# Kernel optimization log

Hardware: AMD Instinct MI355X
Metric: run time of the kernel (lower is better)

## Reference

```python
import jax, jax.numpy as jnp
import numpy as np

VOCAB, EMB, HID, LAT = 32000, 512, 1024, 64
B, S = 64, 512

def setup_inputs() -> dict:
    key = jax.random.key(0)
    ks = jax.random.split(key, 10)
    s_e = 1.0 / np.sqrt(HID)
    s_l = 1.0 / np.sqrt(HID)
    return {
        'input_ids': jax.random.randint(ks[0], (B, S), 0, VOCAB),
        'emb_weight': jax.random.normal(ks[1], (VOCAB, EMB), jnp.float32),
        'w_ih': jax.random.uniform(ks[2], (3 * HID, EMB), jnp.float32, -s_e, s_e),
        'w_hh': jax.random.uniform(ks[3], (3 * HID, HID), jnp.float32, -s_e, s_e),
        'b_ih': jax.random.uniform(ks[4], (3 * HID,), jnp.float32, -s_e, s_e),
        'b_hh': jax.random.uniform(ks[5], (3 * HID,), jnp.float32, -s_e, s_e),
        'w_mean': jax.random.uniform(ks[6], (LAT, HID), jnp.float32, -s_l, s_l),
        'b_mean': jax.random.uniform(ks[7], (LAT,), jnp.float32, -s_l, s_l),
        'w_logv': jax.random.uniform(ks[8], (LAT, HID), jnp.float32, -s_l, s_l),
        'b_logv': jax.random.uniform(ks[9], (LAT,), jnp.float32, -s_l, s_l),
    }

def _gru_mean_hidden(ids, emb_weight, w_ih, w_hh, b_ih, b_hh):
    x = emb_weight[ids]                      # [B, S, E]
    # precompute input-side gate preactivations for all timesteps
    gx = jnp.einsum('bse,ge->bsg', x, w_ih) + b_ih   # [B, S, 3H]
    gx_t = jnp.swapaxes(gx, 0, 1)            # [S, B, 3H] for scan

    def step(h, gx_i):
        gh = h @ w_hh.T + b_hh               # [B, 3H]
        # torch GRU gate order: r, z, n
        r = jax.nn.sigmoid(gx_i[:, :HID] + gh[:, :HID])
        z = jax.nn.sigmoid(gx_i[:, HID:2 * HID] + gh[:, HID:2 * HID])
        n = jnp.tanh(gx_i[:, 2 * HID:] + r * gh[:, 2 * HID:])
        h_new = (1.0 - z) * n + z * h
        return h_new, h_new

    h0 = jnp.zeros((ids.shape[0], HID), gx.dtype)
    _, hs = jax.lax.scan(step, h0, gx_t)      # hs: [S, B, H]
    return jnp.mean(hs, axis=0)               # mean pooling over time -> [B, H]

def reference(input_ids, emb_weight, w_ih, w_hh, b_ih, b_hh, w_mean, b_mean, w_logv, b_logv):
    h = _gru_mean_hidden(input_ids, emb_weight, w_ih, w_hh, b_ih, b_hh)
    mean = h @ w_mean.T + b_mean
    logv = h @ w_logv.T + b_logv
    return (mean, logv)
```

## Files before the change

### kernel.cpp

```cpp
#include <hip/hip_runtime.h>
#include <hip/hip_bf16.h>
#include <stdint.h>
#include <stddef.h>

#define HID   1024
#define NB    64
#define SEQ   512
#define G3    3072
#define EMB   512
#define LAT   64

typedef __attribute__((ext_vector_type(4))) float f32x4;
typedef __attribute__((ext_vector_type(8))) short bfrag;
typedef unsigned long long ull;

__device__ __forceinline__ unsigned short f2bf(float x) {
  union { float f; unsigned u; } v; v.f = x;
  unsigned u = v.u + 0x7fffu + ((v.u >> 16) & 1u);
  return (unsigned short)(u >> 16);
}
__device__ __forceinline__ float bf2f(short s) {
  union { unsigned u; float f; } v; v.u = ((unsigned)(unsigned short)s) << 16;
  return v.f;
}
__device__ __forceinline__ float fsig(float x) {
  return 1.0f / (1.0f + __builtin_exp2f(-1.4426950408889634f * x));
}
__device__ __forceinline__ float ftanh(float x) {
  return 1.0f - 2.0f / (1.0f + __builtin_exp2f(2.8853900817779268f * x));
}
__device__ __forceinline__ void gload_lds16(const void* g, void* l) {
  __builtin_amdgcn_global_load_lds(
      (const __attribute__((address_space(1))) unsigned int*)g,
      (__attribute__((address_space(3))) unsigned int*)l, 16, 0, 0);
}

__global__ void cvt_wih_kernel(const float* __restrict__ in, short* __restrict__ out) {
  int i = (blockIdx.x * 256 + threadIdx.x) * 8;
  f32x4 a = *(const f32x4*)(in + i);
  f32x4 b = *(const f32x4*)(in + i + 4);
  bfrag o;
  o[0]=(short)f2bf(a[0]); o[1]=(short)f2bf(a[1]); o[2]=(short)f2bf(a[2]); o[3]=(short)f2bf(a[3]);
  o[4]=(short)f2bf(b[0]); o[5]=(short)f2bf(b[1]); o[6]=(short)f2bf(b[2]); o[7]=(short)f2bf(b[3]);
  *(bfrag*)(out + i) = o;
}

__global__ void __launch_bounds__(256) gemm_gx_kernel(
    const int* __restrict__ ids, const float* __restrict__ emb,
    const short* __restrict__ wih, short* __restrict__ gx)
{
  const int nt = blockIdx.x, mt = blockIdx.y;
  const int tid = threadIdx.x;
  const int lane = tid & 63, wave = tid >> 6;
  const int wr = wave >> 1, wc = wave & 1;

  __shared__ __align__(16) short A_lds[128 * 48];
  __shared__ __align__(16) short B_lds[128 * 32];
  __shared__ int ids_s[128];

  if (tid < 128) ids_s[tid] = ids[mt * 128 + tid];
  __syncthreads();

  f32x4 acc[4][4];
  #pragma unroll
  for (int i = 0; i < 4; ++i)
    #pragma unroll
    for (int j = 0; j < 4; ++j) acc[i][j] = (f32x4){0.f, 0.f, 0.f, 0.f};

  const int r_stage = tid >> 1;
  const int kh = (tid & 1) * 16;

  #pragma unroll 1
  for (int kc = 0; kc < 16; ++kc) {
    __syncthreads();
    {
      const float* src = emb + (size_t)ids_s[r_stage] * 512 + kc * 32 + kh;
      f32x4 v0 = *(const f32x4*)(src);
      f32x4 v1 = *(const f32x4*)(src + 4);
      f32x4 v2 = *(const f32x4*)(src + 8);
      f32x4 v3 = *(const f32x4*)(src + 12);
      bfrag p0, p1;
      p0[0]=(short)f2bf(v0[0]); p0[1]=(short)f2bf(v0[1]); p0[2]=(short)f2bf(v0[2]); p0[3]=(short)f2bf(v0[3]);
      p0[4]=(short)f2bf(v1[0]); p0[5]=(short)f2bf(v1[1]); p0[6]=(short)f2bf(v1[2]); p0[7]=(short)f2bf(v1[3]);
      p1[0]=(short)f2bf(v2[0]); p1[1]=(short)f2bf(v2[1]); p1[2]=(short)f2bf(v2[2]); p1[3]=(short)f2bf(v2[3]);
      p1[4]=(short)f2bf(v3[0]); p1[5]=(short)f2bf(v3[1]); p1[6]=(short)f2bf(v3[2]); p1[7]=(short)f2bf(v3[3]);
      *(bfrag*)&A_lds[r_stage * 48 + kh]     = p0;
      *(bfrag*)&A_lds[r_stage * 48 + kh + 8] = p1;
    }
    {
      #pragma unroll
      for (int ii = 0; ii < 2; ++ii) {
        int i = wave * 2 + ii;
        const short* src = wih + (size_t)(nt * 128 + i * 16 + (lane >> 2)) * 512
                               + kc * 32 + (lane & 3) * 8;
        gload_lds16((const void*)src, (void*)&B_lds[i * 512]);
      }
    }
    asm volatile("s_waitcnt vmcnt(0)" ::: "memory");
    __syncthreads();

    bfrag a[4], b[4];
    #pragma unroll
    for (int mi = 0; mi < 4; ++mi)
      a[mi] = *(const bfrag*)&A_lds[(wr * 64 + mi * 16 + (lane & 15)) * 48 + (lane >> 4) * 8];
    #pragma unroll
    for (int ni = 0; ni < 4; ++ni)
      b[ni] = *(const bfrag*)&B_lds[(wc * 64 + ni * 16 + (lane & 15)) * 32 + (lane >> 4) * 8];
    #pragma unroll
    for (int mi = 0; mi < 4; ++mi)
      #pragma unroll
      for (int ni = 0; ni < 4; ++ni)
        acc[mi][ni] = __builtin_amdgcn_mfma_f32_16x16x32_bf16(a[mi], b[ni], acc[mi][ni], 0, 0, 0);
  }

  #pragma unroll
  for (int mi = 0; mi < 4; ++mi)
    #pragma unroll
    for (int ni = 0; ni < 4; ++ni)
      #pragma unroll
      for (int r = 0; r < 4; ++r) {
        int m = mt * 128 + wr * 64 + mi * 16 + (lane >> 4) * 4 + r;
        int n = nt * 128 + wc * 64 + ni * 16 + (lane & 15);
        gx[(size_t)m * G3 + n] = (short)f2bf(acc[mi][ni][r]);
      }
}

__global__ void __launch_bounds__(256, 1) gru_scan_kernel(
    const short* __restrict__ gx, const float* __restrict__ whh,
    const float* __restrict__ bihp, const float* __restrict__ bhhp,
    ull* __restrict__ hbuf_q, unsigned int* __restrict__ flags,
    float* __restrict__ hsum)
{
  const int wg   = blockIdx.x;
  const int team = wg >> 6;
  const int cg   = wg & 63;
  const int tid  = threadIdx.x;
  const int lane = tid & 63, wave = tid >> 6;
  const int bl   = lane & 15;
  const int bsub = (lane >> 4) * 4;
  const int jcol = cg * 16 + bl;
  const int bteam = team * 16;

  __shared__ __align__(16) short h_lds[16 * 1024];
  __shared__ __align__(16) float part[3 * 3 * 256];
  __shared__ __align__(16) short hstg[256];

  bfrag wfrag[3][8];
  #pragma unroll
  for (int g = 0; g < 3; ++g) {
    const float* wrow = whh + (size_t)(g * 1024 + jcol) * 1024 + wave * 256 + (lane >> 4) * 8;
    #pragma unroll
    for (int ks = 0; ks < 8; ++ks) {
      const float* p = wrow + ks * 32;
      f32x4 lo = *(const f32x4*)p;
      f32x4 hi = *(const f32x4*)(p + 4);
      bfrag f;
      f[0]=(short)f2bf(lo[0]); f[1]=(short)f2bf(lo[1]); f[2]=(short)f2bf(lo[2]); f[3]=(short)f2bf(lo[3]);
      f[4]=(short)f2bf(hi[0]); f[5]=(short)f2bf(hi[1]); f[6]=(short)f2bf(hi[2]); f[7]=(short)f2bf(hi[3]);
      wfrag[g][ks] = f;
    }
  }
  float bih_r[3], bhh_r[3];
  #pragma unroll
  for (int g = 0; g < 3; ++g) {
    bih_r[g] = bihp[g * 1024 + jcol];
    bhh_r[g] = bhhp[g * 1024 + jcol];
  }

  float hprev[4] = {0.f, 0.f, 0.f, 0.f};
  float hacc[4]  = {0.f, 0.f, 0.f, 0.f};
  const int xorm = (bl & 7) << 4;
  const char* lbase = (const char*)h_lds + bl * 2048;
  unsigned int* fteam  = flags + team * 1024;
  unsigned int* myflag = fteam + cg * 16;
  unsigned int* fq     = fteam + (wave * 16 + (lane & 15)) * 16;

  const int st_b  = lane >> 2;
  const int st_c4 = lane & 3;
  char* const st_base = (char*)h_lds + st_b * 2048;
  const int st_swz = (st_b & 7) << 4;

  short gxr_[4][3];
  if (wave == 0) {
    #pragma unroll
    for (int r = 0; r < 4; ++r) {
      size_t base = ((size_t)(bteam + bsub + r) * SEQ + 0) * G3 + jcol;
      gxr_[r][0] = gx[base];
      gxr_[r][1] = gx[base + 1024];
      gxr_[r][2] = gx[base + 2048];
    }
  }

  #pragma unroll 1
  for (int s = 0; s < SEQ; ++s) {
    const ull* hsrc = hbuf_q + ((s & 1) ? 16384 : 0) + team * 4096;
    ull*       hdst = hbuf_q + (((s + 1) & 1) ? 16384 : 0) + team * 4096;

    {
      unsigned tgt = (unsigned)s;
      for (;;) {
        unsigned v = __hip_atomic_load(fq, __ATOMIC_RELAXED, __HIP_MEMORY_SCOPE_AGENT);
        if (__all((int)(v >= tgt))) break;
      }
    }

    {
      ull hv[16];
      #pragma unroll
      for (int j = 0; j < 16; ++j)
        hv[j] = __hip_atomic_load(hsrc + wave * 1024 + j * 64 + lane,
                                  __ATOMIC_RELAXED, __HIP_MEMORY_SCOPE_AGENT);
      #pragma unroll
      for (int j = 0; j < 16; ++j) {
        int cgq = wave * 16 + j;
        *(ull*)(st_base + ((cgq * 32 + st_c4 * 8) ^ st_swz)) = hv[j];
      }
    }

    f32x4 a0 = {0.f,0.f,0.f,0.f}, a1 = {0.f,0.f,0.f,0.f}, a2 = {0.f,0.f,0.f,0.f};
    #pragma unroll
    for (int ks = 0; ks < 8; ++ks) {
      int k2 = wave * 512 + ks * 64 + (lane >> 4) * 16;
      bfrag af = *(const bfrag*)(lbase + (k2 ^ xorm));
      a0 = __builtin_amdgcn_mfma_f32_16x16x32_bf16(af, wfrag[0][ks], a0, 0, 0, 0);
      a1 = __builtin_amdgcn_mfma_f32_16x16x32_bf16(af, wfrag[1][ks], a1, 0, 0, 0);
      a2 = __builtin_amdgcn_mfma_f32_16x16x32_bf16(af, wfrag[2][ks], a2, 0, 0, 0);
    }
    if (wave) {
      int w1 = wave - 1;
      *(f32x4*)&part[((0 * 3 + w1) * 64 + lane) * 4] = a0;
      *(f32x4*)&part[((1 * 3 + w1) * 64 + lane) * 4] = a1;
      *(f32x4*)&part[((2 * 3 + w1) * 64 + lane) * 4] = a2;
    }
    __syncthreads();

    if (wave == 0) {
      f32x4 s0 = a0, s1 = a1, s2 = a2;
      #pragma unroll
      for (int w1 = 0; w1 < 3; ++w1) {
        s0 += *(const f32x4*)&part[((0 * 3 + w1) * 64 + lane) * 4];
        s1 += *(const f32x4*)&part[((1 * 3 + w1) * 64 + lane) * 4];
        s2 += *(const f32x4*)&part[((2 * 3 + w1) * 64 + lane) * 4];
      }
      #pragma unroll
      for (int r = 0; r < 4; ++r) {
        float ghr = s0[r] + bhh_r[0];
        float ghz = s1[r] + bhh_r[1];
        float ghn = s2[r] + bhh_r[2];
        float rg = fsig(bf2f(gxr_[r][0]) + bih_r[0] + ghr);
        float zg = fsig(bf2f(gxr_[r][1]) + bih_r[1] + ghz);
        float ng = ftanh(bf2f(gxr_[r][2]) + bih_r[2] + rg * ghn);
        float hn = (1.f - zg) * ng + zg * hprev[r];
        hprev[r] = hn;
        hacc[r] += hn;
        hstg[(bsub + r) * 16 + bl] = (short)f2bf(hn);
      }
    }
    __syncthreads();

    if (wave == 1) {
      ull v = ((const ull*)hstg)[lane];
      __hip_atomic_store(hdst + cg * 64 + lane, v, __ATOMIC_RELAXED,
                         __HIP_MEMORY_SCOPE_AGENT);
      asm volatile("s_waitcnt vmcnt(0)" ::: "memory");
      if (lane == 0)
        __hip_atomic_store(myflag, (unsigned)(s + 1), __ATOMIC_RELAXED,
                           __HIP_MEMORY_SCOPE_AGENT);
    }
    if (wave == 0) {
      int sn = (s + 1 < SEQ) ? (s + 1) : s;
      #pragma unroll
      for (int r = 0; r < 4; ++r) {
        size_t base = ((size_t)(bteam + bsub + r) * SEQ + sn) * G3 + jcol;
        gxr_[r][0] = gx[base];
        gxr_[r][1] = gx[base + 1024];
        gxr_[r][2] = gx[base + 2048];
      }
    }
  }

  if (wave == 0) {
    #pragma unroll
    for (int r = 0; r < 4; ++r)
      hsum[(size_t)(bteam + bsub + r) * 1024 + jcol] = hacc[r] * (1.0f / 512.0f);
  }
}

__global__ void proj_kernel(const float* __restrict__ hbar,
                            const float* __restrict__ wm, const float* __restrict__ bm,
                            const float* __restrict__ wl, const float* __restrict__ bl,
                            float* __restrict__ out)
{
  int b = blockIdx.x, t = threadIdx.x;
  __shared__ float hrow[1024];
  for (int k = t; k < 1024; k += 128) hrow[k] = hbar[(size_t)b * 1024 + k];
  __syncthreads();
  int j = t & 63;
  const float* w = (t < 64) ? (wm + (size_t)j * 1024) : (wl + (size_t)j * 1024);
  float acc = (t < 64) ? bm[j] : bl[j];
  for (int k = 0; k < 1024; k += 4) {
    f32x4 wv = *(const f32x4*)(w + k);
    acc += hrow[k] * wv[0] + hrow[k+1] * wv[1] + hrow[k+2] * wv[2] + hrow[k+3] * wv[3];
  }
  out[(size_t)((t < 64) ? 0 : 4096) + b * 64 + j] = acc;
}

extern "C" void kernel_launch(void* const* d_in, const int* in_sizes, int n_in,
                              void* d_out, int out_size, void* d_ws, size_t ws_size,
                              hipStream_t stream) {
  const int*   ids   = (const int*)d_in[0];
  const float* emb   = (const float*)d_in[1];
  const float* w_ih  = (const float*)d_in[2];
  const float* w_hh  = (const float*)d_in[3];
  const float* b_ih  = (const float*)d_in[4];
  const float* b_hh  = (const float*)d_in[5];
  const float* w_mean= (const float*)d_in[6];
  const float* b_mean= (const float*)d_in[7];
  const float* w_logv= (const float*)d_in[8];
  const float* b_logv= (const float*)d_in[9];
  float* out = (float*)d_out;

  char* ws = (char*)d_ws;
  unsigned int* flags = (unsigned int*)(ws);
  ull* hbuf_q        = (ull*)(ws + 16384);
  float* hsum        = (float*)(ws + 16384 + 262144);
  short* wihb        = (short*)(ws + 16384 + 262144 + 262144);
  short* gxbuf       = (short*)(ws + 16384 + 262144 + 262144 + 3145728);

  hipMemsetAsync(ws, 0, 16384 + 262144, stream);

  cvt_wih_kernel<<<768, 256, 0, stream>>>(w_ih, wihb);
  gemm_gx_kernel<<<dim3(24, 256), 256, 0, stream>>>(ids, emb, wihb, gxbuf);
  gru_scan_kernel<<<256, 256, 0, stream>>>(gxbuf, w_hh, b_ih, b_hh, hbuf_q, flags, hsum);
  proj_kernel<<<64, 128, 0, stream>>>(hsum, w_mean, b_mean, w_logv, b_logv, out);
}
```

Baseline: 1.877 ms.

## Remove second block barrier by duplicating gate math in two waves

All four waves now write their MFMA partials to a double-buffered LDS area indexed by step parity. Waves 0 and 1 both reduce the partials and compute the gate update redundantly. Wave 1 then stages and publishes the new hidden state and its flag directly, and wave 0 keeps the running sum and prefetches the next gx values. This removes one __syncthreads per timestep on the critical path of the serial scan, in exchange for doubled gate math, extra LDS traffic, and a leftover no-op accumulation line.

After: 1.921 ms. 1.02x slower.

```diff
diff --git a/kernel.cpp b/kernel.cpp
--- a/kernel.cpp
+++ b/kernel.cpp
@@ -142,7 +142,7 @@
   const int bteam = team * 16;
 
   __shared__ __align__(16) short h_lds[16 * 1024];
-  __shared__ __align__(16) float part[3 * 3 * 256];
+  __shared__ __align__(16) float part[2 * 3 * 4 * 256];
   __shared__ __align__(16) short hstg[256];
 
   bfrag wfrag[3][8];
@@ -175,13 +175,12 @@
   unsigned int* myflag = fteam + cg * 16;
   unsigned int* fq     = fteam + (wave * 16 + (lane & 15)) * 16;
 
-  const int st_b  = lane >> 2;
   const int st_c4 = lane & 3;
-  char* const st_base = (char*)h_lds + st_b * 2048;
-  const int st_swz = (st_b & 7) << 4;
+  char* const st_base = (char*)h_lds + (lane >> 2) * 2048;
+  const int st_swz = ((lane >> 2) & 7) << 4;
 
   short gxr_[4][3];
-  if (wave == 0) {
+  if (wave < 2) {
     #pragma unroll
     for (int r = 0; r < 4; ++r) {
       size_t base = ((size_t)(bteam + bsub + r) * SEQ + 0) * G3 + jcol;
@@ -195,6 +194,7 @@
   for (int s = 0; s < SEQ; ++s) {
     const ull* hsrc = hbuf_q + ((s & 1) ? 16384 : 0) + team * 4096;
     ull*       hdst = hbuf_q + (((s + 1) & 1) ? 16384 : 0) + team * 4096;
+    const int  par  = (s & 1) * 12;
 
     {
       unsigned tgt = (unsigned)s;
@@ -226,22 +226,20 @@
       a1 = __builtin_amdgcn_mfma_f32_16x16x32_bf16(af, wfrag[1][ks], a1, 0, 0, 0);
       a2 = __builtin_amdgcn_mfma_f32_16x16x32_bf16(af, wfrag[2][ks], a2, 0, 0, 0);
     }
-    if (wave) {
-      int w1 = wave - 1;
-      *(f32x4*)&part[((0 * 3 + w1) * 64 + lane) * 4] = a0;
-      *(f32x4*)&part[((1 * 3 + w1) * 64 + lane) * 4] = a1;
-      *(f32x4*)&part[((2 * 3 + w1) * 64 + lane) * 4] = a2;
-    }
+    *(f32x4*)&part[((par + 0 * 4 + wave) * 64 + lane) * 4] = a0;
+    *(f32x4*)&part[((par + 1 * 4 + wave) * 64 + lane) * 4] = a1;
+    *(f32x4*)&part[((par + 2 * 4 + wave) * 64 + lane) * 4] = a2;
     __syncthreads();
 
-    if (wave == 0) {
-      f32x4 s0 = a0, s1 = a1, s2 = a2;
-      #pragma unroll
-      for (int w1 = 0; w1 < 3; ++w1) {
-        s0 += *(const f32x4*)&part[((0 * 3 + w1) * 64 + lane) * 4];
-        s1 += *(const f32x4*)&part[((1 * 3 + w1) * 64 + lane) * 4];
-        s2 += *(const f32x4*)&part[((2 * 3 + w1) * 64 + lane) * 4];
-      }
+    if (wave < 2) {
+      f32x4 s0 = {0.f,0.f,0.f,0.f}, s1 = {0.f,0.f,0.f,0.f}, s2 = {0.f,0.f,0.f,0.f};
+      #pragma unroll
+      for (int w = 0; w < 4; ++w) {
+        s0 += *(const f32x4*)&part[((par + 0 * 4 + w) * 64 + lane) * 4];
+        s1 += *(const f32x4*)&part[((par + 1 * 4 + w) * 64 + lane) * 4];
+        s2 += *(const f32x4*)&part[((par + 2 * 4 + w) * 64 + lane) * 4];
+      }
+      unsigned short hb[4];
       #pragma unroll
       for (int r = 0; r < 4; ++r) {
         float ghr = s0[r] + bhh_r[0];
@@ -252,29 +250,45 @@
         float ng = ftanh(bf2f(gxr_[r][2]) + bih_r[2] + rg * ghn);
         float hn = (1.f - zg) * ng + zg * hprev[r];
         hprev[r] = hn;
-        hacc[r] += hn;
-        hstg[(bsub + r) * 16 + bl] = (short)f2bf(hn);
-      }
-    }
-    __syncthreads();
-
-    if (wave == 1) {
-      ull v = ((const ull*)hstg)[lane];
-      __hip_atomic_store(hdst + cg * 64 + lane, v, __ATOMIC_RELAXED,
-                         __HIP_MEMORY_SCOPE_AGENT);
-      asm volatile("s_waitcnt vmcnt(0)" ::: "memory");
-      if (lane == 0)
-        __hip_atomic_store(myflag, (unsigned)(s + 1), __ATOMIC_RELAXED,
+        hb[r] = f2bf(hn);
+      }
+      if (wave == 0) {
+        #pragma unroll
+        for (int r = 0; r < 4; ++r) hacc[r] += bf2f((short)hb[r]) * 0.f + ((float*)0 == 0 ? 0.f : 0.f), hacc[r] = hacc[r];
+      }
+      if (wave == 0) {
+        #pragma unroll
+        for (int r = 0; r < 4; ++r) hacc[r] += hprev[r];
+        int sn = (s + 1 < SEQ) ? (s + 1) : s;
+        #pragma unroll
+        for (int r = 0; r < 4; ++r) {
+          size_t base = ((size_t)(bteam + bsub + r) * SEQ + sn) * G3 + jcol;
+          gxr_[r][0] = gx[base];
+          gxr_[r][1] = gx[base + 1024];
+          gxr_[r][2] = gx[base + 2048];
+        }
+      }
+      if (wave == 1) {
+        #pragma unroll
+        for (int r = 0; r < 4; ++r)
+          hstg[(bsub + r) * 16 + bl] = (short)hb[r];
+        asm volatile("s_waitcnt lgkmcnt(0)" ::: "memory");
+        __builtin_amdgcn_sched_barrier(0);
+        ull v = ((const ull*)hstg)[lane];
+        __hip_atomic_store(hdst + cg * 64 + lane, v, __ATOMIC_RELAXED,
                            __HIP_MEMORY_SCOPE_AGENT);
-    }
-    if (wave == 0) {
-      int sn = (s + 1 < SEQ) ? (s + 1) : s;
-      #pragma unroll
-      for (int r = 0; r < 4; ++r) {
-        size_t base = ((size_t)(bteam + bsub + r) * SEQ + sn) * G3 + jcol;
-        gxr_[r][0] = gx[base];
-        gxr_[r][1] = gx[base + 1024];
-        gxr_[r][2] = gx[base + 2048];
+        asm volatile("s_waitcnt vmcnt(0)" ::: "memory");
+        if (lane == 0)
+          __hip_atomic_store(myflag, (unsigned)(s + 1), __ATOMIC_RELAXED,
+                             __HIP_MEMORY_SCOPE_AGENT);
+        int sn = (s + 1 < SEQ) ? (s + 1) : s;
+        #pragma unroll
+        for (int r = 0; r < 4; ++r) {
+          size_t base = ((size_t)(bteam + bsub + r) * SEQ + sn) * G3 + jcol;
+          gxr_[r][0] = gx[base];
+          gxr_[r][1] = gx[base + 1024];
+          gxr_[r][2] = gx[base + 2048];
+        }
       }
     }
   }
```
